# Kernel tuning notes

Measured on AMD Instinct MI355X. Metric: run time of the kernel, lower is better.

Reference implementation:

```python
import jax, jax.numpy as jnp
import numpy as np

B, S, H, NH = 2, 2048, 2048, 16
HD = H // NH


def setup_inputs() -> dict:
    key = jax.random.key(0)
    ks = jax.random.split(key, 9)
    s = 1.0 / np.sqrt(H)
    return {
        "hidden_state": jax.random.normal(ks[0], (B, S, H), dtype=jnp.float32),
        "Wq": jax.random.normal(ks[1], (H, H), dtype=jnp.float32) * s,
        "bq": jnp.zeros((H,), dtype=jnp.float32),
        "Wk": jax.random.normal(ks[2], (H, H), dtype=jnp.float32) * s,
        "bk": jnp.zeros((H,), dtype=jnp.float32),
        "Wv": jax.random.normal(ks[3], (H, H), dtype=jnp.float32) * s,
        "bv": jnp.zeros((H,), dtype=jnp.float32),
        "Wo": jax.random.normal(ks[4], (H, H), dtype=jnp.float32) * s,
        "bo": jnp.zeros((H,), dtype=jnp.float32),
    }


def _split_heads(x):
    # [B,S,H] -> [B,NH,S,HD]
    b, s, _ = x.shape
    return x.reshape(b, s, NH, HD).transpose(0, 2, 1, 3)


def reference(hidden_state, Wq, bq, Wk, bk, Wv, bv, Wo, bo):
    q = _split_heads(hidden_state @ Wq.T + bq)
    k = _split_heads(hidden_state @ Wk.T + bk)
    v = _split_heads(hidden_state @ Wv.T + bv)
    scale = 1.0 / jnp.sqrt(jnp.array(HD, dtype=q.dtype))
    scores = jnp.einsum("bhqd,bhkd->bhqk", q, k) * scale
    attn = jax.nn.softmax(scores, axis=-1)
    out = jnp.einsum("bhqk,bhkd->bhqd", attn, v)  # [B,NH,S,HD]
    out = out.transpose(0, 2, 1, 3).reshape(hidden_state.shape[0], -1, H)
    return out @ Wo.T + bo
```

## Files before the change

kernel.cpp:

```cpp
#include <hip/hip_runtime.h>
#include <hip/hip_bf16.h>
#include <stdint.h>

#define B_ 2
#define S_ 2048
#define H_ 2048
#define NH_ 16
#define HD_ 128
#define M_ (B_*S_)

typedef __attribute__((ext_vector_type(8))) short short8_t;
typedef __attribute__((ext_vector_type(4))) float floatx4;

__device__ __forceinline__ short f2bf(float f) {
  union { float f; uint32_t u; } x; x.f = f;
  const uint32_t u = x.u;
  return (short)((u + 0x7FFFu + ((u >> 16) & 1u)) >> 16);
}

__device__ __forceinline__ void gload_lds16(const void* g, void* l) {
  __builtin_amdgcn_global_load_lds(
      (const __attribute__((address_space(1))) void*)g,
      (__attribute__((address_space(3))) void*)l, 16, 0, 0);
}

__global__ __launch_bounds__(256)
void cast_all(const float* __restrict__ h,  const float* __restrict__ wq,
              const float* __restrict__ wk, const float* __restrict__ wv,
              const float* __restrict__ wo,
              short* __restrict__ hB,  short* __restrict__ wqB,
              short* __restrict__ wkB, short* __restrict__ wvB,
              short* __restrict__ woB) {
  const int blk = blockIdx.x;
  const float* src; short* dst; int off;
  if      (blk <  4096) { src = h;  dst = hB;  off = blk; }
  else if (blk <  6144) { src = wq; dst = wqB; off = blk - 4096; }
  else if (blk <  8192) { src = wk; dst = wkB; off = blk - 6144; }
  else if (blk < 10240) { src = wv; dst = wvB; off = blk - 8192; }
  else                  { src = wo; dst = woB; off = blk - 10240; }
  const int i = (off * 256 + threadIdx.x) * 8;
  typedef __attribute__((ext_vector_type(4))) float f4;
  const f4 a = *(const f4*)(src + i);
  const f4 b = *(const f4*)(src + i + 4);
  short8_t o;
  o[0] = f2bf(a[0]); o[1] = f2bf(a[1]); o[2] = f2bf(a[2]); o[3] = f2bf(a[3]);
  o[4] = f2bf(b[0]); o[5] = f2bf(b[1]); o[6] = f2bf(b[2]); o[7] = f2bf(b[3]);
  *(short8_t*)(dst + i) = o;
}

template<bool OUTF32>
__device__ __forceinline__
void gemm_body(const short* __restrict__ A, const short* __restrict__ Bm,
               const float* __restrict__ bias, void* __restrict__ C,
               const int m0, const int n0, const int N, const int K) {
  __shared__ short As[128 * 32];
  __shared__ short Bs[128 * 32];
  const int tid = threadIdx.x;
  const int wv = tid >> 6, ln = tid & 63;
  const int lr = ln >> 4, lc = ln & 15;
  const int wm = (wv >> 1) * 64, wn = (wv & 1) * 64;
  const int srow = ln >> 2, sch = (ln & 3) * 8;

  floatx4 acc[4][4] = {};
  const short* aBase = A  + (size_t)(m0 + srow) * K + sch;
  const short* bBase = Bm + (size_t)(n0 + srow) * K + sch;

  for (int k0 = 0; k0 < K; k0 += 32) {
#pragma unroll
    for (int inst = 0; inst < 2; ++inst) {
      const int rb = inst * 64 + wv * 16;
      gload_lds16(aBase + (size_t)rb * K + k0, &As[rb * 32]);
      gload_lds16(bBase + (size_t)rb * K + k0, &Bs[rb * 32]);
    }
    __syncthreads();
    short8_t af[4], bf[4];
#pragma unroll
    for (int t = 0; t < 4; ++t)
      af[t] = *(const short8_t*)&As[(wm + t * 16 + lc) * 32 + lr * 8];
#pragma unroll
    for (int t = 0; t < 4; ++t)
      bf[t] = *(const short8_t*)&Bs[(wn + t * 16 + lc) * 32 + lr * 8];
#pragma unroll
    for (int i = 0; i < 4; ++i)
#pragma unroll
      for (int j = 0; j < 4; ++j)
        acc[i][j] = __builtin_amdgcn_mfma_f32_16x16x32_bf16(af[i], bf[j], acc[i][j], 0, 0, 0);
    __syncthreads();
  }

#pragma unroll
  for (int i = 0; i < 4; ++i) {
#pragma unroll
    for (int j = 0; j < 4; ++j) {
      const int col = n0 + wn + j * 16 + lc;
      const float bv = bias[col];
#pragma unroll
      for (int r = 0; r < 4; ++r) {
        const int row = m0 + wm + i * 16 + lr * 4 + r;
        const float v = acc[i][j][r] + bv;
        if (OUTF32) ((float*)C)[(size_t)row * N + col] = v;
        else        ((short*)C)[(size_t)row * N + col] = f2bf(v);
      }
    }
  }
}

__global__ __launch_bounds__(256)
void gemm_qkv(const short* __restrict__ A,
              const short* __restrict__ W0, const short* __restrict__ W1, const short* __restrict__ W2,
              const float* __restrict__ b0, const float* __restrict__ b1, const float* __restrict__ b2,
              short* __restrict__ C0, short* __restrict__ C1, short* __restrict__ C2) {
  const int sel = blockIdx.x >> 4;
  const short* Bm   = sel == 0 ? W0 : (sel == 1 ? W1 : W2);
  const float* bias = sel == 0 ? b0 : (sel == 1 ? b1 : b2);
  short* C          = sel == 0 ? C0 : (sel == 1 ? C1 : C2);
  gemm_body<false>(A, Bm, bias, C, blockIdx.y * 128, (blockIdx.x & 15) * 128, H_, H_);
}

__global__ __launch_bounds__(256)
void gemm_out(const short* __restrict__ A, const short* __restrict__ Bm,
              const float* __restrict__ bias, float* __restrict__ C) {
  gemm_body<true>(A, Bm, bias, C, blockIdx.y * 128, blockIdx.x * 128, H_, H_);
}

__global__ __launch_bounds__(256)
void transpose_v(const short* __restrict__ V, short* __restrict__ Vt) {
  __shared__ short T[64][72];
  const int b = blockIdx.z;
  const int s0 = blockIdx.x * 64, c0 = blockIdx.y * 64;
  const int t = threadIdx.x;
  const int r = t >> 3, c8 = (t & 7) * 8;
#pragma unroll
  for (int p = 0; p < 2; ++p) {
    const int row = p * 32 + r;
    *(short8_t*)&T[row][c8] =
        *(const short8_t*)&V[(size_t)(b * S_ + s0 + row) * H_ + c0 + c8];
  }
  __syncthreads();
#pragma unroll
  for (int p = 0; p < 2; ++p) {
    const int row = p * 32 + r;
    short8_t o;
#pragma unroll
    for (int j = 0; j < 8; ++j) o[j] = T[c8 + j][row];
    *(short8_t*)&Vt[(size_t)(b * H_ + c0 + row) * S_ + s0 + c8] = o;
  }
}

__global__ __launch_bounds__(256)
void attention(const short* __restrict__ Q, const short* __restrict__ Kg,
               const short* __restrict__ Vt, short* __restrict__ O) {
  __shared__ short Ks[64 * 136];
  __shared__ short Vs[128 * 72];
  __shared__ short Ps[128 * 72];

  const int tid = threadIdx.x;
  const int wv = tid >> 6, ln = tid & 63;
  const int lr = ln >> 4, lc = ln & 15;
  const int bh = blockIdx.y, b = bh >> 4, h = bh & 15;
  const int q0 = blockIdx.x * 128;

  const short* Qp = Q  + ((size_t)(b * S_ + q0)) * H_ + h * HD_;
  const short* Kp = Kg + (size_t)b * S_ * H_ + h * HD_;
  const short* Vp = Vt + (size_t)bh * HD_ * S_;

  short8_t qf[2][4];
#pragma unroll
  for (int ti = 0; ti < 2; ++ti)
#pragma unroll
    for (int ks = 0; ks < 4; ++ks)
      qf[ti][ks] = *(const short8_t*)&Qp[(size_t)(wv * 32 + ti * 16 + lc) * H_ + ks * 32 + lr * 8];

  floatx4 oacc[2][8] = {};
  float lsum[2][4] = {};

  const float csc = 0.08838834764831845f * 1.4426950408889634f;

  const int krow = tid >> 4, kch = (tid & 15) * 8;
  const int vrow = tid >> 3, vch = (tid & 7) * 8;

  short8_t kreg[4], vreg[4];
#pragma unroll
  for (int p = 0; p < 4; ++p)
    kreg[p] = *(const short8_t*)&Kp[(size_t)(p * 16 + krow) * H_ + kch];
#pragma unroll
  for (int p = 0; p < 4; ++p)
    vreg[p] = *(const short8_t*)&Vp[(size_t)(p * 32 + vrow) * S_ + vch];

  for (int kt = 0; kt < S_ / 64; ++kt) {
    __syncthreads();
#pragma unroll
    for (int p = 0; p < 4; ++p)
      *(short8_t*)&Ks[(p * 16 + krow) * 136 + kch] = kreg[p];
#pragma unroll
    for (int p = 0; p < 4; ++p)
      *(short8_t*)&Vs[(p * 32 + vrow) * 72 + vch] = vreg[p];
    __syncthreads();

    if (kt + 1 < S_ / 64) {
      const int key0 = (kt + 1) * 64;
#pragma unroll
      for (int p = 0; p < 4; ++p)
        kreg[p] = *(const short8_t*)&Kp[(size_t)(key0 + p * 16 + krow) * H_ + kch];
#pragma unroll
      for (int p = 0; p < 4; ++p)
        vreg[p] = *(const short8_t*)&Vp[(size_t)(p * 32 + vrow) * S_ + key0 + vch];
    }

    floatx4 sacc[2][4] = {};
#pragma unroll
    for (int ks = 0; ks < 4; ++ks) {
      short8_t kf[4];
#pragma unroll
      for (int tj = 0; tj < 4; ++tj)
        kf[tj] = *(const short8_t*)&Ks[(tj * 16 + lc) * 136 + ks * 32 + lr * 8];
#pragma unroll
      for (int ti = 0; ti < 2; ++ti)
#pragma unroll
        for (int tj = 0; tj < 4; ++tj)
          sacc[ti][tj] = __builtin_amdgcn_mfma_f32_16x16x32_bf16(qf[ti][ks], kf[tj], sacc[ti][tj], 0, 0, 0);
    }

#pragma unroll
    for (int ti = 0; ti < 2; ++ti) {
#pragma unroll
      for (int r = 0; r < 4; ++r) {
        const int prow = wv * 32 + ti * 16 + lr * 4 + r;
        float acc = 0.f;
#pragma unroll
        for (int tj = 0; tj < 4; ++tj) {
          const float p = exp2f(sacc[ti][tj][r] * csc);
          acc += p;
          Ps[prow * 72 + tj * 16 + lc] = f2bf(p);
        }
        lsum[ti][r] += acc;
      }
    }

#pragma unroll
    for (int ks = 0; ks < 2; ++ks) {
      short8_t pf[2];
#pragma unroll
      for (int ti = 0; ti < 2; ++ti)
        pf[ti] = *(const short8_t*)&Ps[(wv * 32 + ti * 16 + lc) * 72 + ks * 32 + lr * 8];
#pragma unroll
      for (int tj = 0; tj < 8; ++tj) {
        const short8_t vf = *(const short8_t*)&Vs[(tj * 16 + lc) * 72 + ks * 32 + lr * 8];
#pragma unroll
        for (int ti = 0; ti < 2; ++ti)
          oacc[ti][tj] = __builtin_amdgcn_mfma_f32_16x16x32_bf16(pf[ti], vf, oacc[ti][tj], 0, 0, 0);
      }
    }
  }

  short* Op = O + ((size_t)(b * S_ + q0)) * H_ + h * HD_;
#pragma unroll
  for (int ti = 0; ti < 2; ++ti) {
#pragma unroll
    for (int r = 0; r < 4; ++r) {
      float l = lsum[ti][r];
      l += __shfl_xor(l, 1);
      l += __shfl_xor(l, 2);
      l += __shfl_xor(l, 4);
      l += __shfl_xor(l, 8);
      const float inv = 1.0f / l;
      const int row = wv * 32 + ti * 16 + lr * 4 + r;
#pragma unroll
      for (int tj = 0; tj < 8; ++tj)
        Op[(size_t)row * H_ + tj * 16 + lc] = f2bf(oacc[ti][tj][r] * inv);
    }
  }
}

extern "C" void kernel_launch(void* const* d_in, const int* in_sizes, int n_in,
                              void* d_out, int out_size, void* d_ws, size_t ws_size,
                              hipStream_t stream) {
  const float* hidden = (const float*)d_in[0];
  const float* Wq = (const float*)d_in[1];
  const float* bq = (const float*)d_in[2];
  const float* Wk = (const float*)d_in[3];
  const float* bk = (const float*)d_in[4];
  const float* Wv = (const float*)d_in[5];
  const float* bv = (const float*)d_in[6];
  const float* Wo = (const float*)d_in[7];
  const float* bo = (const float*)d_in[8];
  float* out = (float*)d_out;

  char* ws = (char*)d_ws;
  short* hB  = (short*)(ws);
  short* WqB = (short*)(ws + (16u << 20));
  short* WkB = (short*)(ws + (24u << 20));
  short* WvB = (short*)(ws + (32u << 20));
  short* WoB = (short*)(ws + (40u << 20));
  short* Qb  = (short*)(ws + (48u << 20));
  short* Kb  = (short*)(ws + (64u << 20));
  short* Vb  = (short*)(ws + (80u << 20));
  short* Vtb = (short*)(ws + (96u << 20));
  short* Ob  = (short*)(ws + (112u << 20));

  cast_all<<<12288, 256, 0, stream>>>(hidden, Wq, Wk, Wv, Wo, hB, WqB, WkB, WvB, WoB);

  gemm_qkv<<<dim3(48, M_ / 128), 256, 0, stream>>>(hB, WqB, WkB, WvB, bq, bk, bv, Qb, Kb, Vb);

  transpose_v<<<dim3(S_ / 64, H_ / 64, B_), 256, 0, stream>>>(Vb, Vtb);

  attention<<<dim3(S_ / 128, B_ * NH_), 256, 0, stream>>>(Qb, Kb, Vtb, Ob);

  gemm_out<<<dim3(H_ / 128, M_ / 128), 256, 0, stream>>>(Ob, WoB, bo, out);
}
```

Before: 449.5 us.

## Pre-tile K/V into swizzled per-head blocks and load attention tiles via LDS DMA

The QKV GEMM now writes K directly in a per-head, per-64-key tiled layout with an XOR swizzle, and the V transpose kernel emits V^T in the same tiled, swizzled form. Attention then streams each K/V tile into unpadded LDS with global_load_lds instead of register staging. It moves to 512 threads per block, 16 query rows per wave, and a swizzled P buffer. The P row sum now uses the truncated bf16 value and exp is converted by truncation rather than rounding. This drops the register prefetch, so loads no longer overlap compute and precision shifts slightly.

After: 428.9 us. -4.6%, faster.

```diff
diff --git a/kernel.cpp b/kernel.cpp
--- a/kernel.cpp
+++ b/kernel.cpp
@@ -48,7 +48,7 @@
   *(short8_t*)(dst + i) = o;
 }
 
-template<bool OUTF32>
+template<int MODE>
 __device__ __forceinline__
 void gemm_body(const short* __restrict__ A, const short* __restrict__ Bm,
                const float* __restrict__ bias, void* __restrict__ C,
@@ -98,8 +98,17 @@
       for (int r = 0; r < 4; ++r) {
         const int row = m0 + wm + i * 16 + lr * 4 + r;
         const float v = acc[i][j][r] + bv;
-        if (OUTF32) ((float*)C)[(size_t)row * N + col] = v;
-        else        ((short*)C)[(size_t)row * N + col] = f2bf(v);
+        if (MODE == 1) {
+          ((float*)C)[(size_t)row * N + col] = v;
+        } else if (MODE == 0) {
+          ((short*)C)[(size_t)row * N + col] = f2bf(v);
+        } else {
+          const int bb = row >> 11, s = row & 2047;
+          const int kt = s >> 6, key = s & 63;
+          const int hh = col >> 7, d = col & 127;
+          const int cp = d ^ ((key & 7) << 3);
+          ((short*)C)[((((size_t)(bb * 16 + hh) * 32 + kt) * 64 + key) << 7) + cp] = f2bf(v);
+        }
       }
     }
   }
@@ -111,25 +120,26 @@
               const float* __restrict__ b0, const float* __restrict__ b1, const float* __restrict__ b2,
               short* __restrict__ C0, short* __restrict__ C1, short* __restrict__ C2) {
   const int sel = blockIdx.x >> 4;
-  const short* Bm   = sel == 0 ? W0 : (sel == 1 ? W1 : W2);
-  const float* bias = sel == 0 ? b0 : (sel == 1 ? b1 : b2);
-  short* C          = sel == 0 ? C0 : (sel == 1 ? C1 : C2);
-  gemm_body<false>(A, Bm, bias, C, blockIdx.y * 128, (blockIdx.x & 15) * 128, H_, H_);
+  const int n0 = (blockIdx.x & 15) * 128, m0 = blockIdx.y * 128;
+  if (sel == 0)      gemm_body<0>(A, W0, b0, C0, m0, n0, H_, H_);
+  else if (sel == 1) gemm_body<2>(A, W1, b1, C1, m0, n0, H_, H_);
+  else               gemm_body<0>(A, W2, b2, C2, m0, n0, H_, H_);
 }
 
 __global__ __launch_bounds__(256)
 void gemm_out(const short* __restrict__ A, const short* __restrict__ Bm,
               const float* __restrict__ bias, float* __restrict__ C) {
-  gemm_body<true>(A, Bm, bias, C, blockIdx.y * 128, blockIdx.x * 128, H_, H_);
-}
-
-__global__ __launch_bounds__(256)
-void transpose_v(const short* __restrict__ V, short* __restrict__ Vt) {
+  gemm_body<1>(A, Bm, bias, C, blockIdx.y * 128, blockIdx.x * 128, H_, H_);
+}
+
+__global__ __launch_bounds__(256)
+void arrange_v(const short* __restrict__ V, short* __restrict__ Vt) {
   __shared__ short T[64][72];
   const int b = blockIdx.z;
   const int s0 = blockIdx.x * 64, c0 = blockIdx.y * 64;
   const int t = threadIdx.x;
   const int r = t >> 3, c8 = (t & 7) * 8;
+  const int kt = s0 >> 6;
 #pragma unroll
   for (int p = 0; p < 2; ++p) {
     const int row = p * 32 + r;
@@ -140,135 +150,101 @@
 #pragma unroll
   for (int p = 0; p < 2; ++p) {
     const int row = p * 32 + r;
+    const int gcol = c0 + row;
+    const int hh = gcol >> 7, d = gcol & 127;
     short8_t o;
 #pragma unroll
     for (int j = 0; j < 8; ++j) o[j] = T[c8 + j][row];
-    *(short8_t*)&Vt[(size_t)(b * H_ + c0 + row) * S_ + s0 + c8] = o;
-  }
-}
-
-__global__ __launch_bounds__(256)
-void attention(const short* __restrict__ Q, const short* __restrict__ Kg,
+    const int chunk = (c8 >> 3) ^ (d & 7);
+    *(short8_t*)&Vt[((((size_t)(b * 16 + hh) * 32 + kt) * 128 + d) << 6) + chunk * 8] = o;
+  }
+}
+
+__global__ __launch_bounds__(512, 4)
+void attention(const short* __restrict__ Q, const short* __restrict__ Kt,
                const short* __restrict__ Vt, short* __restrict__ O) {
-  __shared__ short Ks[64 * 136];
-  __shared__ short Vs[128 * 72];
-  __shared__ short Ps[128 * 72];
+  __shared__ short Ks[64 * 128];
+  __shared__ short Vs[128 * 64];
+  __shared__ short Ps[128 * 64];
 
   const int tid = threadIdx.x;
   const int wv = tid >> 6, ln = tid & 63;
   const int lr = ln >> 4, lc = ln & 15;
   const int bh = blockIdx.y, b = bh >> 4, h = bh & 15;
-  const int q0 = blockIdx.x * 128;
-
-  const short* Qp = Q  + ((size_t)(b * S_ + q0)) * H_ + h * HD_;
-  const short* Kp = Kg + (size_t)b * S_ * H_ + h * HD_;
-  const short* Vp = Vt + (size_t)bh * HD_ * S_;
-
-  short8_t qf[2][4];
-#pragma unroll
-  for (int ti = 0; ti < 2; ++ti)
-#pragma unroll
-    for (int ks = 0; ks < 4; ++ks)
-      qf[ti][ks] = *(const short8_t*)&Qp[(size_t)(wv * 32 + ti * 16 + lc) * H_ + ks * 32 + lr * 8];
-
-  floatx4 oacc[2][8] = {};
-  float lsum[2][4] = {};
-
+  const int qw = blockIdx.x * 128 + wv * 16;
+
+  const short* Qp  = Q  + ((size_t)(b * S_ + qw)) * H_ + h * HD_;
+  const short* KtB = Kt + (size_t)bh * (S_ * HD_);
+  const short* VtB = Vt + (size_t)bh * (S_ * HD_);
+
+  short8_t qf[4];
+#pragma unroll
+  for (int ksq = 0; ksq < 4; ++ksq)
+    qf[ksq] = *(const short8_t*)&Qp[(size_t)lc * H_ + ksq * 32 + lr * 8];
+
+  floatx4 oacc[8] = {};
+  float lsum[4] = {};
   const float csc = 0.08838834764831845f * 1.4426950408889634f;
-
-  const int krow = tid >> 4, kch = (tid & 15) * 8;
-  const int vrow = tid >> 3, vch = (tid & 7) * 8;
-
-  short8_t kreg[4], vreg[4];
-#pragma unroll
-  for (int p = 0; p < 4; ++p)
-    kreg[p] = *(const short8_t*)&Kp[(size_t)(p * 16 + krow) * H_ + kch];
-#pragma unroll
-  for (int p = 0; p < 4; ++p)
-    vreg[p] = *(const short8_t*)&Vp[(size_t)(p * 32 + vrow) * S_ + vch];
+  const int sA = (lc & 7) << 3;
+  const int i0 = wv * 1024 + ln * 8;
 
   for (int kt = 0; kt < S_ / 64; ++kt) {
-    __syncthreads();
-#pragma unroll
-    for (int p = 0; p < 4; ++p)
-      *(short8_t*)&Ks[(p * 16 + krow) * 136 + kch] = kreg[p];
-#pragma unroll
-    for (int p = 0; p < 4; ++p)
-      *(short8_t*)&Vs[(p * 32 + vrow) * 72 + vch] = vreg[p];
-    __syncthreads();
-
-    if (kt + 1 < S_ / 64) {
-      const int key0 = (kt + 1) * 64;
-#pragma unroll
-      for (int p = 0; p < 4; ++p)
-        kreg[p] = *(const short8_t*)&Kp[(size_t)(key0 + p * 16 + krow) * H_ + kch];
-#pragma unroll
-      for (int p = 0; p < 4; ++p)
-        vreg[p] = *(const short8_t*)&Vp[(size_t)(p * 32 + vrow) * S_ + key0 + vch];
-    }
-
-    floatx4 sacc[2][4] = {};
-#pragma unroll
-    for (int ks = 0; ks < 4; ++ks) {
-      short8_t kf[4];
-#pragma unroll
-      for (int tj = 0; tj < 4; ++tj)
-        kf[tj] = *(const short8_t*)&Ks[(tj * 16 + lc) * 136 + ks * 32 + lr * 8];
-#pragma unroll
-      for (int ti = 0; ti < 2; ++ti)
-#pragma unroll
-        for (int tj = 0; tj < 4; ++tj)
-          sacc[ti][tj] = __builtin_amdgcn_mfma_f32_16x16x32_bf16(qf[ti][ks], kf[tj], sacc[ti][tj], 0, 0, 0);
-    }
-
-#pragma unroll
-    for (int ti = 0; ti < 2; ++ti) {
+    const size_t tb = (size_t)kt * 8192;
+    gload_lds16(KtB + tb + i0,       &Ks[wv * 1024]);
+    gload_lds16(KtB + tb + i0 + 512, &Ks[wv * 1024 + 512]);
+    gload_lds16(VtB + tb + i0,       &Vs[wv * 1024]);
+    gload_lds16(VtB + tb + i0 + 512, &Vs[wv * 1024 + 512]);
+    __syncthreads();
+
+    floatx4 sacc[4] = {};
+#pragma unroll
+    for (int ksq = 0; ksq < 4; ++ksq) {
+#pragma unroll
+      for (int tj = 0; tj < 4; ++tj) {
+        const short8_t kf =
+            *(const short8_t*)&Ks[(tj * 16 + lc) * 128 + ((ksq * 32 + lr * 8) ^ sA)];
+        sacc[tj] = __builtin_amdgcn_mfma_f32_16x16x32_bf16(qf[ksq], kf, sacc[tj], 0, 0, 0);
+      }
+    }
+
+#pragma unroll
+    for (int tj = 0; tj < 4; ++tj) {
 #pragma unroll
       for (int r = 0; r < 4; ++r) {
-        const int prow = wv * 32 + ti * 16 + lr * 4 + r;
-        float acc = 0.f;
-#pragma unroll
-        for (int tj = 0; tj < 4; ++tj) {
-          const float p = exp2f(sacc[ti][tj][r] * csc);
-          acc += p;
-          Ps[prow * 72 + tj * 16 + lc] = f2bf(p);
-        }
-        lsum[ti][r] += acc;
+        const float p = exp2f(sacc[tj][r] * csc);
+        const uint32_t u = __float_as_uint(p);
+        const int row = wv * 16 + lr * 4 + r;
+        Ps[row * 64 + ((tj * 16 + lc) ^ ((row & 7) << 3))] = (short)(u >> 16);
+        lsum[r] += __uint_as_float(u & 0xffff0000u);
       }
     }
 
 #pragma unroll
     for (int ks = 0; ks < 2; ++ks) {
-      short8_t pf[2];
-#pragma unroll
-      for (int ti = 0; ti < 2; ++ti)
-        pf[ti] = *(const short8_t*)&Ps[(wv * 32 + ti * 16 + lc) * 72 + ks * 32 + lr * 8];
+      const short8_t pf =
+          *(const short8_t*)&Ps[(wv * 16 + lc) * 64 + ((ks * 32 + lr * 8) ^ sA)];
 #pragma unroll
       for (int tj = 0; tj < 8; ++tj) {
-        const short8_t vf = *(const short8_t*)&Vs[(tj * 16 + lc) * 72 + ks * 32 + lr * 8];
-#pragma unroll
-        for (int ti = 0; ti < 2; ++ti)
-          oacc[ti][tj] = __builtin_amdgcn_mfma_f32_16x16x32_bf16(pf[ti], vf, oacc[ti][tj], 0, 0, 0);
-      }
-    }
-  }
-
-  short* Op = O + ((size_t)(b * S_ + q0)) * H_ + h * HD_;
-#pragma unroll
-  for (int ti = 0; ti < 2; ++ti) {
-#pragma unroll
-    for (int r = 0; r < 4; ++r) {
-      float l = lsum[ti][r];
-      l += __shfl_xor(l, 1);
-      l += __shfl_xor(l, 2);
-      l += __shfl_xor(l, 4);
-      l += __shfl_xor(l, 8);
-      const float inv = 1.0f / l;
-      const int row = wv * 32 + ti * 16 + lr * 4 + r;
-#pragma unroll
-      for (int tj = 0; tj < 8; ++tj)
-        Op[(size_t)row * H_ + tj * 16 + lc] = f2bf(oacc[ti][tj][r] * inv);
-    }
+        const short8_t vf =
+            *(const short8_t*)&Vs[(tj * 16 + lc) * 64 + ((ks * 32 + lr * 8) ^ sA)];
+        oacc[tj] = __builtin_amdgcn_mfma_f32_16x16x32_bf16(pf, vf, oacc[tj], 0, 0, 0);
+      }
+    }
+    __syncthreads();
+  }
+
+  short* Op = O + ((size_t)(b * S_ + qw)) * H_ + h * HD_;
+#pragma unroll
+  for (int r = 0; r < 4; ++r) {
+    float l = lsum[r];
+    l += __shfl_xor(l, 1);
+    l += __shfl_xor(l, 2);
+    l += __shfl_xor(l, 4);
+    l += __shfl_xor(l, 8);
+    const float inv = 1.0f / l;
+#pragma unroll
+    for (int tj = 0; tj < 8; ++tj)
+      Op[(size_t)(lr * 4 + r) * H_ + tj * 16 + lc] = f2bf(oacc[tj][r] * inv);
   }
 }
 
@@ -293,18 +269,18 @@
   short* WvB = (short*)(ws + (32u << 20));
   short* WoB = (short*)(ws + (40u << 20));
   short* Qb  = (short*)(ws + (48u << 20));
-  short* Kb  = (short*)(ws + (64u << 20));
+  short* Ktb = (short*)(ws + (64u << 20));
   short* Vb  = (short*)(ws + (80u << 20));
   short* Vtb = (short*)(ws + (96u << 20));
   short* Ob  = (short*)(ws + (112u << 20));
 
   cast_all<<<12288, 256, 0, stream>>>(hidden, Wq, Wk, Wv, Wo, hB, WqB, WkB, WvB, WoB);
 
-  gemm_qkv<<<dim3(48, M_ / 128), 256, 0, stream>>>(hB, WqB, WkB, WvB, bq, bk, bv, Qb, Kb, Vb);
-
-  transpose_v<<<dim3(S_ / 64, H_ / 64, B_), 256, 0, stream>>>(Vb, Vtb);
-
-  attention<<<dim3(S_ / 128, B_ * NH_), 256, 0, stream>>>(Qb, Kb, Vtb, Ob);
+  gemm_qkv<<<dim3(48, M_ / 128), 256, 0, stream>>>(hB, WqB, WkB, WvB, bq, bk, bv, Qb, Ktb, Vb);
+
+  arrange_v<<<dim3(S_ / 64, H_ / 64, B_), 256, 0, stream>>>(Vb, Vtb);
+
+  attention<<<dim3(S_ / 128, B_ * NH_), 512, 0, stream>>>(Qb, Ktb, Vtb, Ob);
 
   gemm_out<<<dim3(H_ / 128, M_ / 128), 256, 0, stream>>>(Ob, WoB, bo, out);
 }
```
